# Kernel tuning notes

Measured on AMD Instinct MI355X. Metric: run time of the kernel, lower is better.

Reference implementation:

```python
import jax, jax.numpy as jnp
import numpy as np

ALPHA = 0.2  # leaky-relu slope (relu_a)
EPS = 1e-16  # guard for isolated nodes (matches pyGAT div-by-rowsum semantics up to eps)


def sp_gat_layer(x, row, col, W, a1, a2, concat):
    # pyGAT sparse attention layer (eval mode, no dropout).
    N = x.shape[0]
    h = x @ W                                   # [N, F_out]
    # a @ [h_src || h_dst] decomposed to avoid materializing edge_h [E, 2F]
    logits = h[row] @ a1 + h[col] @ a2          # [E]
    e = jnp.exp(-jax.nn.leaky_relu(logits, ALPHA))
    rowsum = jax.ops.segment_sum(e, row, num_segments=N)                 # [N]
    hp = jax.ops.segment_sum(e[:, None] * h[col], row, num_segments=N)  # [N, F_out]
    hp = hp / (rowsum[:, None] + EPS)
    return jax.nn.elu(hp) if concat else hp


def setup_inputs() -> dict:
    key = jax.random.key(0)
    ks = jax.random.split(key, 12)
    N, E = 50000, 800000
    nfeat, nhid, nclass, nstruc, nheads = 256, 32, 40, 128, 8
    hid = nhid * nheads  # 256

    def xav(k, shape):
        fan = shape[-2] + shape[-1]
        return jax.random.uniform(k, shape, jnp.float32, -1.0, 1.0) * jnp.sqrt(6.0 / fan)

    x = jax.random.normal(ks[0], (N, nfeat), jnp.float32)
    edge_index = jax.random.randint(ks[1], (2, E), 0, N, jnp.int32)
    W_att = xav(ks[2], (nheads, nfeat, nhid))
    a1 = jax.random.normal(ks[3], (nheads, nhid), jnp.float32) * 0.1
    a2 = jax.random.normal(ks[4], (nheads, nhid), jnp.float32) * 0.1
    W_out = xav(ks[5], (hid, nclass))
    a1_out = jax.random.normal(ks[6], (nclass,), jnp.float32) * 0.1
    a2_out = jax.random.normal(ks[7], (nclass,), jnp.float32) * 0.1
    W_gc = xav(ks[8], (hid, hid))
    b_gc = jnp.zeros((hid,), jnp.float32)
    W_enc = xav(ks[9], (hid, nstruc))
    b_enc = jnp.zeros((nstruc,), jnp.float32)
    return dict(x=x, edge_index=edge_index, W_att=W_att, a1=a1, a2=a2,
                W_out=W_out, a1_out=a1_out, a2_out=a2_out,
                W_gc=W_gc, b_gc=b_gc, W_enc=W_enc, b_enc=b_enc)


def reference(x, edge_index, W_att, a1, a2, W_out, a1_out, a2_out, W_gc, b_gc, W_enc, b_enc):
    N = x.shape[0]
    row, col = edge_index[0], edge_index[1]
    nheads = W_att.shape[0]
    # multi-head sparse attention, concat (loop over fixed small head count)
    heads = [sp_gat_layer(x, row, col, W_att[i], a1[i], a2[i], True) for i in range(nheads)]
    h1 = jnp.concatenate(heads, axis=1)                 # [N, nhid*nheads]
    # GraphConvolution: adj @ (h1 @ W) + b  (binary adjacency from edge list)
    support = h1 @ W_gc                                 # [N, hid]
    h2 = jax.ops.segment_sum(support[col], row, num_segments=N) + b_gc
    # output attention head (concat=False) then elu
    xo = jax.nn.elu(sp_gat_layer(h2, row, col, W_out, a1_out, a2_out, False))
    y = h1 @ W_enc + b_enc
    z = h2 @ W_enc + b_enc
    return (jax.nn.log_softmax(xo, axis=1), y, z)
```

## Files before the change

kernel.cpp:

```cpp
#include <hip/hip_runtime.h>
#include <math.h>

typedef __attribute__((ext_vector_type(8))) short short8;
typedef __attribute__((ext_vector_type(4))) ushort u16x4;
typedef __attribute__((ext_vector_type(8))) ushort u16x8;
typedef __attribute__((ext_vector_type(8))) __bf16 bf16x8;
typedef __attribute__((ext_vector_type(4))) float f32x4;

#define LOG2E 1.44269504088896f

__device__ inline ushort f2bf(float x) {
  union { float f; unsigned u; } v; v.f = x;
  unsigned r = v.u + 0x7fff + ((v.u >> 16) & 1);
  return (ushort)(r >> 16);
}
__device__ inline float bf2f(ushort b) {
  union { unsigned u; float f; } v; v.u = (unsigned)b << 16; return v.f;
}

#define GLOAD_LDS16(g, l)                                                      \
  __builtin_amdgcn_global_load_lds(                                            \
      (const __attribute__((address_space(1))) void*)(g),                      \
      (__attribute__((address_space(3))) void*)(l), 16, 0, 0)

__device__ inline void pack_one(float val, int k, int n, int Fp, ushort* __restrict__ dst) {
  int kb = k >> 5, kr = k & 31;
  int lane = ((kr >> 3) << 4) | (n & 15);
  int j = kr & 7;
  int nb = n >> 4;
  size_t off = ((size_t)(kb * (Fp / 16) + nb) * 64 + lane) * 8 + j;
  dst[off] = f2bf(val);
}

__global__ void pack_all(const float* __restrict__ W_att, const float* __restrict__ W_gc,
                         const float* __restrict__ W_enc, const float* __restrict__ W_out,
                         const float* __restrict__ a1o, const float* __restrict__ a2o,
                         ushort* __restrict__ Bp, ushort* __restrict__ Wg,
                         ushort* __restrict__ We, ushort* __restrict__ Wo) {
  int tid = blockIdx.x * blockDim.x + threadIdx.x;
  if (tid < 65536) {
    int k = tid >> 8, n = tid & 255;
    float val = W_att[(size_t)(n >> 5) * 8192 + k * 32 + (n & 31)];
    pack_one(val, k, n, 256, Bp);
  } else if (tid < 131072) {
    int t2 = tid - 65536;
    int k = t2 >> 8, n = t2 & 255;
    pack_one(W_gc[k * 256 + n], k, n, 256, Wg);
  } else if (tid < 163840) {
    int t2 = tid - 131072;
    int k = t2 >> 7, n = t2 & 127;
    pack_one(W_enc[k * 128 + n], k, n, 128, We);
  } else if (tid < 180224) {
    int t2 = tid - 163840;
    int k = t2 >> 6, n = t2 & 63;
    float val;
    if (n < 40) {
      val = W_out[k * 40 + n];
    } else if (n == 40) {
      val = 0.f;
      for (int j = 0; j < 40; ++j) val = fmaf(W_out[k * 40 + j], a1o[j], val);
    } else if (n == 41) {
      val = 0.f;
      for (int j = 0; j < 40; ++j) val = fmaf(W_out[k * 40 + j], a2o[j], val);
    } else {
      val = 0.f;
    }
    pack_one(val, k, n, 64, Wo);
  }
}

template <int Fp, int F, int OUTMODE, bool BIAS, bool BFIN, bool SOUT>
__global__ __launch_bounds__(512) void gemm_mfma(const float* __restrict__ A,
                                                 const ushort* __restrict__ Ab,
                                                 const ushort* __restrict__ Bp,
                                                 const float* __restrict__ bias,
                                                 float* __restrict__ C,
                                                 ushort* __restrict__ Cb,
                                                 float* __restrict__ s1o,
                                                 float* __restrict__ s2o, int Nv, int NPAD) {
  constexpr int NB = Fp / 64;
  __shared__ ushort lhs[64 * 256];
  int n0 = blockIdx.x * 64;
  int t = threadIdx.x;
  int wv = t >> 6, l = t & 63;
  if (BFIN) {
#pragma unroll
    for (int i = 0; i < 4; ++i) {
      int u = i * 512 + wv * 64 + l;
      int r = u >> 5, cs = u & 31;
      int csrc = cs ^ (r & 7);
      const ushort* src = Ab + (size_t)(n0 + r) * 256 + csrc * 8;
      GLOAD_LDS16(src, lhs + (size_t)(i * 512 + wv * 64) * 8);
    }
  } else {
    int r = t >> 3, q = t & 7;
    int row = n0 + r;
    bool rin = row < Nv;
#pragma unroll
    for (int i = 0; i < 4; ++i) {
      int c0 = q * 32 + i * 8;
      int c8 = (c0 >> 3) ^ (r & 7);
      float4 f0 = {0.f, 0.f, 0.f, 0.f}, f1 = {0.f, 0.f, 0.f, 0.f};
      if (rin) {
        f0 = *reinterpret_cast<const float4*>(A + (size_t)row * 256 + c0);
        f1 = *reinterpret_cast<const float4*>(A + (size_t)row * 256 + c0 + 4);
      }
      float ff[8] = {f0.x, f0.y, f0.z, f0.w, f1.x, f1.y, f1.z, f1.w};
      short8 sh;
#pragma unroll
      for (int j = 0; j < 8; ++j) sh[j] = (short)f2bf(ff[j]);
      *reinterpret_cast<short8*>(&lhs[r * 256 + c8 * 8]) = sh;
    }
  }
  __syncthreads();
  int wr = wv >> 2, wc = wv & 3;
  int lr = l & 15, lk = l >> 4;
  f32x4 acc[2][NB];
#pragma unroll
  for (int m = 0; m < 2; ++m)
#pragma unroll
    for (int nb = 0; nb < NB; ++nb) acc[m][nb] = (f32x4){0.f, 0.f, 0.f, 0.f};

#pragma unroll
  for (int ks = 0; ks < 8; ++ks) {
    bf16x8 ah[2];
#pragma unroll
    for (int m = 0; m < 2; ++m) {
      int row = wr * 32 + m * 16 + lr;
      int c8 = (ks * 4 + lk) ^ (row & 7);
      ah[m] = *reinterpret_cast<const bf16x8*>(&lhs[row * 256 + c8 * 8]);
    }
#pragma unroll
    for (int nb = 0; nb < NB; ++nb) {
      size_t off = ((size_t)(ks * (Fp / 16) + wc * NB + nb) * 64 + l) * 8;
      bf16x8 bh = *reinterpret_cast<const bf16x8*>(&Bp[off]);
#pragma unroll
      for (int m = 0; m < 2; ++m)
        acc[m][nb] = __builtin_amdgcn_mfma_f32_16x16x32_bf16(ah[m], bh, acc[m][nb], 0, 0, 0);
    }
  }
#pragma unroll
  for (int m = 0; m < 2; ++m) {
    int rowbase = n0 + wr * 32 + m * 16 + lk * 4;
#pragma unroll
    for (int nb = 0; nb < NB; ++nb) {
      int col = wc * (NB * 16) + nb * 16 + lr;
#pragma unroll
      for (int rg = 0; rg < 4; ++rg) {
        int gr = rowbase + rg;
        int crow;
        bool ok;
        if (NPAD == 0) {
          crow = gr; ok = gr < Nv;
        } else if (gr < NPAD) {
          crow = gr; ok = gr < Nv;
        } else {
          int g2 = gr - NPAD;
          crow = Nv + g2; ok = g2 < Nv;
        }
        if (ok) {
          float v = acc[m][nb][rg];
          if (col < F) {
            if (BIAS) v += bias[col];
            if (OUTMODE != 2) C[(size_t)crow * F + col] = v;
            if (OUTMODE != 0) Cb[(size_t)crow * F + col] = f2bf(v);
          } else if (SOUT && col == 40) {
            s1o[crow] = v;
          } else if (SOUT && col == 41) {
            s2o[crow] = v;
          }
        }
      }
    }
  }
}

__global__ void calc_s12(const ushort* __restrict__ Hb, const float* __restrict__ a1,
                         const float* __restrict__ a2, float* __restrict__ s1,
                         float* __restrict__ s2, int N) {
  int tid = blockIdx.x * blockDim.x + threadIdx.x;
  if (tid >= N * 8) return;
  int h = tid & 7;
  int n = tid >> 3;
  const ushort* hp = Hb + (size_t)n * 256 + h * 32;
  const float* A1 = a1 + h * 32;
  const float* A2 = a2 + h * 32;
  float d1 = 0.f, d2 = 0.f;
#pragma unroll
  for (int j0 = 0; j0 < 32; j0 += 8) {
    u16x8 hv = *reinterpret_cast<const u16x8*>(hp + j0);
#pragma unroll
    for (int j = 0; j < 8; ++j) {
      float v = bf2f(hv[j]);
      d1 = fmaf(v, A1[j0 + j], d1);
      d2 = fmaf(v, A2[j0 + j], d2);
    }
  }
  s1[tid] = d1;
  s2[tid] = d2;
}

__global__ void hist_deg(const int* __restrict__ row, int* __restrict__ deg, int E) {
  int e = blockIdx.x * blockDim.x + threadIdx.x;
  if (e < E) atomicAdd(&deg[row[e]], 1);
}

__global__ void scan1(const int* __restrict__ deg, int* __restrict__ rp, int* __restrict__ bsum,
                      int N) {
  __shared__ int sd[256];
  int t = threadIdx.x;
  int i = blockIdx.x * 256 + t;
  int v = (i < N) ? deg[i] : 0;
  sd[t] = v;
  __syncthreads();
  for (int off = 1; off < 256; off <<= 1) {
    int x = (t >= off) ? sd[t - off] : 0;
    __syncthreads();
    sd[t] += x;
    __syncthreads();
  }
  if (i < N) rp[i] = sd[t] - v;
  if (t == 255) bsum[blockIdx.x] = sd[255];
}

__global__ void scan2(int* __restrict__ bsum, int nb) {
  __shared__ int sd[256];
  int t = threadIdx.x;
  int v = (t < nb) ? bsum[t] : 0;
  sd[t] = v;
  __syncthreads();
  for (int off = 1; off < 256; off <<= 1) {
    int x = (t >= off) ? sd[t - off] : 0;
    __syncthreads();
    sd[t] += x;
    __syncthreads();
  }
  if (t < nb) bsum[t] = sd[t] - v;
}

__global__ void scan3(int* __restrict__ rp, const int* __restrict__ bsum, int N, int E) {
  int i = blockIdx.x * 256 + threadIdx.x;
  if (i < N) rp[i] += bsum[blockIdx.x];
  if (i == 0) rp[N] = E;
}

__global__ void scatter_edges(const int* __restrict__ row, const int* __restrict__ col,
                              const int* __restrict__ rp, int* __restrict__ cur,
                              int* __restrict__ scol, int* __restrict__ srow, int E) {
  int e = blockIdx.x * blockDim.x + threadIdx.x;
  if (e >= E) return;
  int r = row[e];
  int p = atomicAdd(&cur[r], 1);
  int idx = rp[r] + p;
  scol[idx] = col[e];
  srow[idx] = r;
}

__global__ void edge_wo(const int* __restrict__ srow, const int* __restrict__ scol,
                        const float* __restrict__ s1o, const float* __restrict__ s2o,
                        float* __restrict__ wo, int E) {
  int e = blockIdx.x * blockDim.x + threadIdx.x;
  if (e >= E) return;
  float lg = s1o[srow[e]] + s2o[scol[e]];
  float lr = lg > 0.f ? lg : 0.2f * lg;
  wo[e] = __builtin_amdgcn_exp2f(-LOG2E * lr);
}

__global__ __launch_bounds__(64) void agg_att(const ushort* __restrict__ Hb,
                                              const float* __restrict__ s1,
                                              const float* __restrict__ s2,
                                              const int* __restrict__ rp,
                                              const int* __restrict__ scol,
                                              ushort* __restrict__ h1b, int N) {
  int n = blockIdx.x;
  int t = threadIdx.x;
  int head = t >> 3;
  float s1n = s1[n * 8 + head];
  float acc[4] = {0.f, 0.f, 0.f, 0.f};
  float rs = 0.f;
  int beg = rp[n], end = rp[n + 1];
  for (int i = beg; i < end; ++i) {
    int c = scol[i];
    float lg = s1n + s2[c * 8 + head];
    float lr = lg > 0.f ? lg : 0.2f * lg;
    float wv = __builtin_amdgcn_exp2f(-LOG2E * lr);
    rs += wv;
    const u16x4 hv = *reinterpret_cast<const u16x4*>(Hb + (size_t)c * 256 + t * 4);
#pragma unroll
    for (int j = 0; j < 4; ++j) acc[j] = fmaf(wv, bf2f(hv[j]), acc[j]);
  }
  float inv = 1.f / (rs + 1e-16f);
  u16x4 ov;
#pragma unroll
  for (int j = 0; j < 4; ++j) {
    float v = acc[j] * inv;
    v = v > 0.f ? v : expm1f(v);
    ov[j] = f2bf(v);
  }
  *reinterpret_cast<u16x4*>(h1b + (size_t)n * 256 + t * 4) = ov;
}

__global__ __launch_bounds__(64) void agg_gc(const ushort* __restrict__ Sb,
                                             const int* __restrict__ rp,
                                             const int* __restrict__ scol,
                                             const float* __restrict__ b_gc,
                                             ushort* __restrict__ h2b, int N) {
  int n = blockIdx.x;
  int t = threadIdx.x;
  float acc[4] = {0.f, 0.f, 0.f, 0.f};
  int beg = rp[n], end = rp[n + 1];
  for (int i = beg; i < end; ++i) {
    int c = scol[i];
    const u16x4 sv = *reinterpret_cast<const u16x4*>(Sb + (size_t)c * 256 + t * 4);
#pragma unroll
    for (int j = 0; j < 4; ++j) acc[j] += bf2f(sv[j]);
  }
  const float4 bv = *reinterpret_cast<const float4*>(b_gc + t * 4);
  float o[4] = {acc[0] + bv.x, acc[1] + bv.y, acc[2] + bv.z, acc[3] + bv.w};
  u16x4 ov;
#pragma unroll
  for (int j = 0; j < 4; ++j) ov[j] = f2bf(o[j]);
  *reinterpret_cast<u16x4*>(h2b + (size_t)n * 256 + t * 4) = ov;
}

__global__ __launch_bounds__(64) void agg_out_lsm(const ushort* __restrict__ Hob,
                                                  const float* __restrict__ wo,
                                                  const int* __restrict__ rp,
                                                  const int* __restrict__ scol,
                                                  float* __restrict__ out0, int N) {
  int n = blockIdx.x;
  int t = threadIdx.x;
  float acc = 0.f, rs = 0.f;
  int beg = rp[n], end = rp[n + 1];
  for (int i = beg; i < end; ++i) {
    int c = scol[i];
    float wv = wo[i];
    rs += wv;
    if (t < 40) acc = fmaf(wv, bf2f(Hob[(size_t)c * 40 + t]), acc);
  }
  float hp = acc / (rs + 1e-16f);
  float xo = (t < 40) ? (hp > 0.f ? hp : expm1f(hp)) : -3.0e38f;
  float mx = xo;
#pragma unroll
  for (int m = 1; m < 64; m <<= 1) mx = fmaxf(mx, __shfl_xor(mx, m));
  float ex = (t < 40) ? expf(xo - mx) : 0.f;
  float sum = ex;
#pragma unroll
  for (int m = 1; m < 64; m <<= 1) sum += __shfl_xor(sum, m);
  if (t < 40) out0[(size_t)n * 40 + t] = xo - mx - logf(sum);
}

extern "C" void kernel_launch(void* const* d_in, const int* in_sizes, int n_in,
                              void* d_out, int out_size, void* d_ws, size_t ws_size,
                              hipStream_t stream) {
  const float* x      = (const float*)d_in[0];
  const int*   ei     = (const int*)d_in[1];
  const float* W_att  = (const float*)d_in[2];
  const float* a1     = (const float*)d_in[3];
  const float* a2     = (const float*)d_in[4];
  const float* W_out  = (const float*)d_in[5];
  const float* a1_out = (const float*)d_in[6];
  const float* a2_out = (const float*)d_in[7];
  const float* W_gc   = (const float*)d_in[8];
  const float* b_gc   = (const float*)d_in[9];
  const float* W_enc  = (const float*)d_in[10];
  const float* b_enc  = (const float*)d_in[11];

  const int N = in_sizes[0] / 256;
  const int E = in_sizes[1] / 2;
  const int N64 = (N + 63) & ~63;
  const int* row = ei;
  const int* col = ei + E;

  char* p = (char*)d_ws;
  auto alloc = [&](size_t bytes) -> void* {
    void* r = (void*)p;
    p += (bytes + 255) & ~(size_t)255;
    return r;
  };
  ushort* hbuf = (ushort*)alloc((size_t)N64 * 256 * 2);
  ushort* h1b  = (ushort*)alloc((size_t)2 * N64 * 256 * 2);
  ushort* h2b  = h1b + (size_t)N64 * 256;
  ushort* Hob = (ushort*)alloc((size_t)N * 40 * 2);
  float* s1   = (float*)alloc((size_t)N * 8 * 4);
  float* s2   = (float*)alloc((size_t)N * 8 * 4);
  float* s1o  = (float*)alloc((size_t)N * 4);
  float* s2o  = (float*)alloc((size_t)N * 4);
  int* deg    = (int*)alloc((size_t)2 * N * 4);
  int* cur    = deg + N;
  int* rp     = (int*)alloc((size_t)(N + 1) * 4);
  int* bsum   = (int*)alloc(256 * 4);
  int* scol   = (int*)alloc((size_t)E * 4);
  int* srow   = (int*)alloc((size_t)E * 4);
  float* wo   = (float*)alloc((size_t)E * 4);
  ushort* Bp  = (ushort*)alloc((size_t)65536 * 2);
  ushort* Wg  = (ushort*)alloc((size_t)65536 * 2);
  ushort* We  = (ushort*)alloc((size_t)32768 * 2);
  ushort* Wo  = (ushort*)alloc((size_t)16384 * 2);

  float* out0 = (float*)d_out;
  float* outY = out0 + (size_t)N * 40;

  const int nb = (N + 255) / 256;
  const int gblk = N64 / 64;
  const int gblk2 = 2 * N64 / 64;

  pack_all<<<dim3((180224 + 255) / 256), dim3(256), 0, stream>>>(
      W_att, W_gc, W_enc, W_out, a1_out, a2_out, Bp, Wg, We, Wo);

  hipMemsetAsync(deg, 0, (size_t)2 * N * 4, stream);
  hist_deg<<<dim3((E + 255) / 256), dim3(256), 0, stream>>>(row, deg, E);
  scan1<<<dim3(nb), dim3(256), 0, stream>>>(deg, rp, bsum, N);
  scan2<<<dim3(1), dim3(256), 0, stream>>>(bsum, nb);
  scan3<<<dim3(nb), dim3(256), 0, stream>>>(rp, bsum, N, E);
  scatter_edges<<<dim3((E + 255) / 256), dim3(256), 0, stream>>>(row, col, rp, cur, scol, srow, E);

  gemm_mfma<256, 256, 2, false, false, false><<<dim3(gblk), dim3(512), 0, stream>>>(
      x, nullptr, Bp, nullptr, nullptr, hbuf, nullptr, nullptr, N, 0);
  calc_s12<<<dim3((N * 8 + 255) / 256), dim3(256), 0, stream>>>(hbuf, a1, a2, s1, s2, N);
  agg_att<<<dim3(N), dim3(64), 0, stream>>>(hbuf, s1, s2, rp, scol, h1b, N);

  gemm_mfma<256, 256, 2, false, true, false><<<dim3(gblk), dim3(512), 0, stream>>>(
      nullptr, h1b, Wg, nullptr, nullptr, hbuf, nullptr, nullptr, N, 0);
  agg_gc<<<dim3(N), dim3(64), 0, stream>>>(hbuf, rp, scol, b_gc, h2b, N);

  gemm_mfma<64, 40, 2, false, true, true><<<dim3(gblk), dim3(512), 0, stream>>>(
      nullptr, h2b, Wo, nullptr, nullptr, Hob, s1o, s2o, N, 0);
  edge_wo<<<dim3((E + 255) / 256), dim3(256), 0, stream>>>(srow, scol, s1o, s2o, wo, E);
  agg_out_lsm<<<dim3(N), dim3(64), 0, stream>>>(Hob, wo, rp, scol, out0, N);

  gemm_mfma<128, 128, 0, true, true, false><<<dim3(gblk2), dim3(512), 0, stream>>>(
      nullptr, h1b, We, b_enc, outY, nullptr, nullptr, nullptr, N, N64);
}
```

Baseline: 389.4 us.

## Fuse W_enc projections into W_gc and W_out GEMMs; pack four nodes per block

The W_enc projections for y and z are folded into the existing GEMMs by concatenating weight matrices: W_gc||W_enc for h1 (384 columns) and W_out+attention columns||W_enc for h2 (192 columns). This drops the separate encoder GEMM launch and avoids re-reading h1b/h2b from memory. The aggregation kernels now run four 64-thread wavefronts per 256-thread block instead of one wavefront per block, which reduces the block count. The cost is wider per-block GEMM tiles with more accumulators, which can lower occupancy.

```diff
diff --git a/kernel.cpp b/kernel.cpp
--- a/kernel.cpp
+++ b/kernel.cpp
@@ -35,24 +35,21 @@
 __global__ void pack_all(const float* __restrict__ W_att, const float* __restrict__ W_gc,
                          const float* __restrict__ W_enc, const float* __restrict__ W_out,
                          const float* __restrict__ a1o, const float* __restrict__ a2o,
-                         ushort* __restrict__ Bp, ushort* __restrict__ Wg,
-                         ushort* __restrict__ We, ushort* __restrict__ Wo) {
+                         ushort* __restrict__ Bp, ushort* __restrict__ WgWe,
+                         ushort* __restrict__ WoWe) {
   int tid = blockIdx.x * blockDim.x + threadIdx.x;
   if (tid < 65536) {
     int k = tid >> 8, n = tid & 255;
     float val = W_att[(size_t)(n >> 5) * 8192 + k * 32 + (n & 31)];
     pack_one(val, k, n, 256, Bp);
-  } else if (tid < 131072) {
+  } else if (tid < 65536 + 98304) {
     int t2 = tid - 65536;
-    int k = t2 >> 8, n = t2 & 255;
-    pack_one(W_gc[k * 256 + n], k, n, 256, Wg);
-  } else if (tid < 163840) {
-    int t2 = tid - 131072;
-    int k = t2 >> 7, n = t2 & 127;
-    pack_one(W_enc[k * 128 + n], k, n, 128, We);
-  } else if (tid < 180224) {
-    int t2 = tid - 163840;
-    int k = t2 >> 6, n = t2 & 63;
+    int k = t2 / 384, n = t2 % 384;
+    float val = (n < 256) ? W_gc[k * 256 + n] : W_enc[k * 128 + (n - 256)];
+    pack_one(val, k, n, 384, WgWe);
+  } else if (tid < 65536 + 98304 + 49152) {
+    int t2 = tid - 65536 - 98304;
+    int k = t2 / 192, n = t2 % 192;
     float val;
     if (n < 40) {
       val = W_out[k * 40 + n];
@@ -62,14 +59,16 @@
     } else if (n == 41) {
       val = 0.f;
       for (int j = 0; j < 40; ++j) val = fmaf(W_out[k * 40 + j], a2o[j], val);
+    } else if (n < 64) {
+      val = 0.f;
     } else {
-      val = 0.f;
-    }
-    pack_one(val, k, n, 64, Wo);
-  }
-}
-
-template <int Fp, int F, int OUTMODE, bool BIAS, bool BFIN, bool SOUT>
+      val = W_enc[k * 128 + (n - 64)];
+    }
+    pack_one(val, k, n, 192, WoWe);
+  }
+}
+
+template <int Fp, int MODE>
 __global__ __launch_bounds__(512) void gemm_mfma(const float* __restrict__ A,
                                                  const ushort* __restrict__ Ab,
                                                  const ushort* __restrict__ Bp,
@@ -77,13 +76,13 @@
                                                  float* __restrict__ C,
                                                  ushort* __restrict__ Cb,
                                                  float* __restrict__ s1o,
-                                                 float* __restrict__ s2o, int Nv, int NPAD) {
+                                                 float* __restrict__ s2o, int Nv) {
   constexpr int NB = Fp / 64;
   __shared__ ushort lhs[64 * 256];
   int n0 = blockIdx.x * 64;
   int t = threadIdx.x;
   int wv = t >> 6, l = t & 63;
-  if (BFIN) {
+  if (MODE != 0) {
 #pragma unroll
     for (int i = 0; i < 4; ++i) {
       int u = i * 512 + wv * 64 + l;
@@ -148,26 +147,25 @@
 #pragma unroll
       for (int rg = 0; rg < 4; ++rg) {
         int gr = rowbase + rg;
-        int crow;
-        bool ok;
-        if (NPAD == 0) {
-          crow = gr; ok = gr < Nv;
-        } else if (gr < NPAD) {
-          crow = gr; ok = gr < Nv;
+        if (gr >= Nv) continue;
+        float v = acc[m][nb][rg];
+        if (MODE == 0) {
+          Cb[(size_t)gr * 256 + col] = f2bf(v);
+        } else if (MODE == 1) {
+          if (col < 256) {
+            Cb[(size_t)gr * 256 + col] = f2bf(v);
+          } else {
+            C[(size_t)gr * 128 + (col - 256)] = v + bias[col - 256];
+          }
         } else {
-          int g2 = gr - NPAD;
-          crow = Nv + g2; ok = g2 < Nv;
-        }
-        if (ok) {
-          float v = acc[m][nb][rg];
-          if (col < F) {
-            if (BIAS) v += bias[col];
-            if (OUTMODE != 2) C[(size_t)crow * F + col] = v;
-            if (OUTMODE != 0) Cb[(size_t)crow * F + col] = f2bf(v);
-          } else if (SOUT && col == 40) {
-            s1o[crow] = v;
-          } else if (SOUT && col == 41) {
-            s2o[crow] = v;
+          if (col < 40) {
+            Cb[(size_t)gr * 40 + col] = f2bf(v);
+          } else if (col == 40) {
+            s1o[gr] = v;
+          } else if (col == 41) {
+            s2o[gr] = v;
+          } else if (col >= 64) {
+            C[(size_t)gr * 128 + (col - 64)] = v + bias[col - 64];
           }
         }
       }
@@ -266,14 +264,15 @@
   wo[e] = __builtin_amdgcn_exp2f(-LOG2E * lr);
 }
 
-__global__ __launch_bounds__(64) void agg_att(const ushort* __restrict__ Hb,
-                                              const float* __restrict__ s1,
-                                              const float* __restrict__ s2,
-                                              const int* __restrict__ rp,
-                                              const int* __restrict__ scol,
-                                              ushort* __restrict__ h1b, int N) {
-  int n = blockIdx.x;
-  int t = threadIdx.x;
+__global__ __launch_bounds__(256) void agg_att(const ushort* __restrict__ Hb,
+                                               const float* __restrict__ s1,
+                                               const float* __restrict__ s2,
+                                               const int* __restrict__ rp,
+                                               const int* __restrict__ scol,
+                                               ushort* __restrict__ h1b, int N) {
+  int n = blockIdx.x * 4 + (threadIdx.x >> 6);
+  if (n >= N) return;
+  int t = threadIdx.x & 63;
   int head = t >> 3;
   float s1n = s1[n * 8 + head];
   float acc[4] = {0.f, 0.f, 0.f, 0.f};
@@ -300,13 +299,14 @@
   *reinterpret_cast<u16x4*>(h1b + (size_t)n * 256 + t * 4) = ov;
 }
 
-__global__ __launch_bounds__(64) void agg_gc(const ushort* __restrict__ Sb,
-                                             const int* __restrict__ rp,
-                                             const int* __restrict__ scol,
-                                             const float* __restrict__ b_gc,
-                                             ushort* __restrict__ h2b, int N) {
-  int n = blockIdx.x;
-  int t = threadIdx.x;
+__global__ __launch_bounds__(256) void agg_gc(const ushort* __restrict__ Sb,
+                                              const int* __restrict__ rp,
+                                              const int* __restrict__ scol,
+                                              const float* __restrict__ b_gc,
+                                              ushort* __restrict__ h2b, int N) {
+  int n = blockIdx.x * 4 + (threadIdx.x >> 6);
+  if (n >= N) return;
+  int t = threadIdx.x & 63;
   float acc[4] = {0.f, 0.f, 0.f, 0.f};
   int beg = rp[n], end = rp[n + 1];
   for (int i = beg; i < end; ++i) {
@@ -323,13 +323,14 @@
   *reinterpret_cast<u16x4*>(h2b + (size_t)n * 256 + t * 4) = ov;
 }
 
-__global__ __launch_bounds__(64) void agg_out_lsm(const ushort* __restrict__ Hob,
-                                                  const float* __restrict__ wo,
-                                                  const int* __restrict__ rp,
-                                                  const int* __restrict__ scol,
-                                                  float* __restrict__ out0, int N) {
-  int n = blockIdx.x;
-  int t = threadIdx.x;
+__global__ __launch_bounds__(256) void agg_out_lsm(const ushort* __restrict__ Hob,
+                                                   const float* __restrict__ wo,
+                                                   const int* __restrict__ rp,
+                                                   const int* __restrict__ scol,
+                                                   float* __restrict__ out0, int N) {
+  int n = blockIdx.x * 4 + (threadIdx.x >> 6);
+  if (n >= N) return;
+  int t = threadIdx.x & 63;
   float acc = 0.f, rs = 0.f;
   int beg = rp[n], end = rp[n + 1];
   for (int i = beg; i < end; ++i) {
@@ -379,8 +380,8 @@
     return r;
   };
   ushort* hbuf = (ushort*)alloc((size_t)N64 * 256 * 2);
-  ushort* h1b  = (ushort*)alloc((size_t)2 * N64 * 256 * 2);
-  ushort* h2b  = h1b + (size_t)N64 * 256;
+  ushort* h1b  = (ushort*)alloc((size_t)N64 * 256 * 2);
+  ushort* h2b  = (ushort*)alloc((size_t)N64 * 256 * 2);
   ushort* Hob = (ushort*)alloc((size_t)N * 40 * 2);
   float* s1   = (float*)alloc((size_t)N * 8 * 4);
   float* s2   = (float*)alloc((size_t)N * 8 * 4);
@@ -393,20 +394,19 @@
   int* scol   = (int*)alloc((size_t)E * 4);
   int* srow   = (int*)alloc((size_t)E * 4);
   float* wo   = (float*)alloc((size_t)E * 4);
-  ushort* Bp  = (ushort*)alloc((size_t)65536 * 2);
-  ushort* Wg  = (ushort*)alloc((size_t)65536 * 2);
-  ushort* We  = (ushort*)alloc((size_t)32768 * 2);
-  ushort* Wo  = (ushort*)alloc((size_t)16384 * 2);
+  ushort* Bp   = (ushort*)alloc((size_t)65536 * 2);
+  ushort* WgWe = (ushort*)alloc((size_t)98304 * 2);
+  ushort* WoWe = (ushort*)alloc((size_t)49152 * 2);
 
   float* out0 = (float*)d_out;
   float* outY = out0 + (size_t)N * 40;
+  float* outZ = outY + (size_t)N * 128;
 
   const int nb = (N + 255) / 256;
   const int gblk = N64 / 64;
-  const int gblk2 = 2 * N64 / 64;
-
-  pack_all<<<dim3((180224 + 255) / 256), dim3(256), 0, stream>>>(
-      W_att, W_gc, W_enc, W_out, a1_out, a2_out, Bp, Wg, We, Wo);
+
+  pack_all<<<dim3((212992 + 255) / 256), dim3(256), 0, stream>>>(
+      W_att, W_gc, W_enc, W_out, a1_out, a2_out, Bp, WgWe, WoWe);
 
   hipMemsetAsync(deg, 0, (size_t)2 * N * 4, stream);
   hist_deg<<<dim3((E + 255) / 256), dim3(256), 0, stream>>>(row, deg, E);
@@ -415,20 +415,17 @@
   scan3<<<dim3(nb), dim3(256), 0, stream>>>(rp, bsum, N, E);
   scatter_edges<<<dim3((E + 255) / 256), dim3(256), 0, stream>>>(row, col, rp, cur, scol, srow, E);
 
-  gemm_mfma<256, 256, 2, false, false, false><<<dim3(gblk), dim3(512), 0, stream>>>(
-      x, nullptr, Bp, nullptr, nullptr, hbuf, nullptr, nullptr, N, 0);
+  gemm_mfma<256, 0><<<dim3(gblk), dim3(512), 0, stream>>>(
+      x, nullptr, Bp, nullptr, nullptr, hbuf, nullptr, nullptr, N);
   calc_s12<<<dim3((N * 8 + 255) / 256), dim3(256), 0, stream>>>(hbuf, a1, a2, s1, s2, N);
-  agg_att<<<dim3(N), dim3(64), 0, stream>>>(hbuf, s1, s2, rp, scol, h1b, N);
-
-  gemm_mfma<256, 256, 2, false, true, false><<<dim3(gblk), dim3(512), 0, stream>>>(
-      nullptr, h1b, Wg, nullptr, nullptr, hbuf, nullptr, nullptr, N, 0);
-  agg_gc<<<dim3(N), dim3(64), 0, stream>>>(hbuf, rp, scol, b_gc, h2b, N);
-
-  gemm_mfma<64, 40, 2, false, true, true><<<dim3(gblk), dim3(512), 0, stream>>>(
-      nullptr, h2b, Wo, nullptr, nullptr, Hob, s1o, s2o, N, 0);
+  agg_att<<<dim3((N + 3) / 4), dim3(256), 0, stream>>>(hbuf, s1, s2, rp, scol, h1b, N);
+
+  gemm_mfma<384, 1><<<dim3(gblk), dim3(512), 0, stream>>>(
+      nullptr, h1b, WgWe, b_enc, outY, hbuf, nullptr, nullptr, N);
+  agg_gc<<<dim3((N + 3) / 4), dim3(256), 0, stream>>>(hbuf, rp, scol, b_gc, h2b, N);
+
+  gemm_mfma<192, 2><<<dim3(gblk), dim3(512), 0, stream>>>(
+      nullptr, h2b, WoWe, b_enc, outZ, Hob, s1o, s2o, N);
   edge_wo<<<dim3((E + 255) / 256), dim3(256), 0, stream>>>(srow, scol, s1o, s2o, wo, E);
-  agg_out_lsm<<<dim3(N), dim3(64), 0, stream>>>(Hob, wo, rp, scol, out0, N);
-
-  gemm_mfma<128, 128, 0, true, true, false><<<dim3(gblk2), dim3(512), 0, stream>>>(
-      nullptr, h1b, We, b_enc, outY, nullptr, nullptr, nullptr, N, N64);
-}
+  agg_out_lsm<<<dim3((N + 3) / 4), dim3(256), 0, stream>>>(Hob, wo, rp, scol, out0, N);
+}
```

Result: slower. 477.4 us (+22.6%).
